# Kernel tuning notes

Hardware: AMD Instinct MI355X
Metric: run time of the kernel (lower is better)

Reference implementation:

```python
import jax, jax.numpy as jnp
import numpy as np

N, C, RATIO, POS_P = 8192, 5000, 3.0, 0.01


def setup_inputs() -> dict:
    key = jax.random.key(0)
    k1, k2 = jax.random.split(key)
    pred = jax.random.normal(k1, (N, C), dtype=jnp.float32)
    # sparse binary multilabel targets (~50 positives per row)
    target = (jax.random.uniform(k2, (N, C)) < POS_P).astype(jnp.float32)
    return {"pred": pred, "target": target}


def reference(pred, target):
    # pred, target: [N, C]
    num_classes = pred.shape[-1]
    pos = jnp.sum(target, axis=-1)                         # [N] positives per row
    neg = jnp.minimum(pos * RATIO, num_classes - pos)      # [N] hard negatives to keep

    # hard-negative selection: top-neg entries of softmax(pred) - target
    prob = jax.nn.softmax(pred, axis=-1)
    score = prob - target                                  # positives pushed below negatives
    # rank 0 = largest score (matches torch.topk ordering)
    ranks = jnp.argsort(jnp.argsort(-score, axis=-1), axis=-1)
    hard = (ranks < neg[:, None]).astype(pred.dtype)       # [N, C]
    mask = jnp.maximum(target, hard)                       # mask = target.clone(); mask[topk]=1

    # old-torch multilabel_soft_margin_loss(size_average=False) == weighted BCE sum:
    # -(y*log sigmoid(x) + (1-y)*log(1-sigmoid(x))) = softplus(x) - y*x
    bce = jax.nn.softplus(pred) - target * pred
    loss = jnp.sum(mask * bce)
    return loss / jnp.sum(target)
```

## Files before the change

### kernel.cpp

```cpp
#include <hip/hip_runtime.h>
#include <stdint.h>


#define C_DIM 5000
#define C4_DIM 1250
#define BLK 256
#define SCAP 1024
#define PCAP 512
#define CUT 1.25f
#define NSLOT 64

__device__ __forceinline__ float sp_f(float x) {
    return fmaxf(x, 0.0f) + __logf(1.0f + __expf(-fabsf(x)));
}
__device__ __forceinline__ uint32_t mono_u(float x) {
    uint32_t b = __float_as_uint(x);
    return b ^ ((b & 0x80000000u) ? 0xFFFFFFFFu : 0x80000000u);
}
__device__ __forceinline__ float unmono_f(uint32_t u) {
    uint32_t b = (u & 0x80000000u) ? (u ^ 0x80000000u) : ~u;
    return __uint_as_float(b);
}
__device__ __forceinline__ int vbin_of(float x) {
    int v = (int)((x - CUT) * 128.0f);
    return v > 255 ? 255 : (v < 0 ? 0 : v);
}

__device__ __forceinline__ void find_bin(const unsigned int* hist, int kp, int tid, int* s_sel) {
    if (tid < 64) {
        int c0 = (int)hist[4 * tid + 0];
        int c1 = (int)hist[4 * tid + 1];
        int c2 = (int)hist[4 * tid + 2];
        int c3 = (int)hist[4 * tid + 3];
        int lsum = c0 + c1 + c2 + c3;
        int s = lsum;
        #pragma unroll
        for (int off = 1; off < 64; off <<= 1) {
            int o = __shfl_down(s, off);
            if (tid + off < 64) s += o;
        }
        int above = s - lsum;
        if (above < kp && kp <= s) {
            int b, ab;
            if (kp <= above + c3)                { b = 4 * tid + 3; ab = above; }
            else if (kp <= above + c3 + c2)      { b = 4 * tid + 2; ab = above + c3; }
            else if (kp <= above + c3 + c2 + c1) { b = 4 * tid + 1; ab = above + c3 + c2; }
            else                                 { b = 4 * tid;     ab = above + c3 + c2 + c1; }
            s_sel[0] = b;
            s_sel[1] = ab;
        }
    }
}

__global__ __launch_bounds__(BLK, 4) void hardneg_kernel(
    const float* __restrict__ pred, const float* __restrict__ target,
    char* __restrict__ ws)
{
    __shared__ uint32_t s_buf[SCAP];
    __shared__ uint32_t s_pbuf[PCAP];
    __shared__ unsigned int hist[256];
    __shared__ float f_scr[4];
    __shared__ int s_sel[2];
    __shared__ int s_misc[4];
    __shared__ int s_cnt;
    __shared__ int s_pcnt;
    __shared__ uint32_t s_tiny[64];

    const int tid = threadIdx.x;
    const int lane = tid & 63;
    const int wv = tid >> 6;
    const int row = blockIdx.x;
    const float4* pr4 = (const float4*)(pred + (size_t)row * C_DIM);
    const float4* tg4 = (const float4*)(target + (size_t)row * C_DIM);

    hist[tid] = 0;
    if (tid < 4) s_misc[tid] = 0;
    if (tid == 0) { s_cnt = 0; s_pcnt = 0; }
    __syncthreads();

    #pragma unroll
    for (int c = 0; c < 5; ++c) {
        int i = tid + c * BLK;
        if (c < 4 || i < C4_DIM) {
            float4 p = pr4[i];
            float4 t = tg4[i];
            float xs[4] = {p.x, p.y, p.z, p.w};
            float ts[4] = {t.x, t.y, t.z, t.w};
            #pragma unroll
            for (int j = 0; j < 4; ++j) {
                float x = xs[j];
                if (ts[j] != 0.0f) {
                    int ip = atomicAdd(&s_pcnt, 1);
                    if (ip < PCAP) s_pbuf[ip] = __float_as_uint(x);
                } else if (x > CUT) {
                    int ic = atomicAdd(&s_cnt, 1);
                    if (ic < SCAP) s_buf[ic] = __float_as_uint(x) ^ 0x80000000u;
                }
            }
        }
    }
    __syncthreads();

    const int pos_total = s_pcnt;
    const int cnt = s_cnt;
    const int k = min(3 * pos_total, C_DIM - pos_total);
    if (k == 0) return;

    float acc = 0.0f;
    if (pos_total <= PCAP) {
        for (int i = tid; i < pos_total; i += BLK) {
            float x = __uint_as_float(s_pbuf[i]);
            acc += sp_f(x) - x;
        }
    } else {
        for (int i = tid; i < C4_DIM; i += BLK) {
            float4 p = pr4[i];
            float4 t = tg4[i];
            float xs[4] = {p.x, p.y, p.z, p.w};
            float ts[4] = {t.x, t.y, t.z, t.w};
            #pragma unroll
            for (int j = 0; j < 4; ++j)
                if (ts[j] != 0.0f) acc += sp_f(xs[j]) - xs[j];
        }
    }

    uint32_t tu;
    int n_at;
    const bool fb = (k > cnt) || (cnt > SCAP);

    if (!fb) {
        for (int i = tid; i < cnt; i += BLK)
            atomicAdd(&hist[vbin_of(unmono_f(s_buf[i]))], 1u);
        __syncthreads();
        find_bin(hist, k, tid, s_sel);
        __syncthreads();
        const int bv = s_sel[0];
        int kp = k - s_sel[1];

        for (int i = tid; i < cnt; i += BLK) {
            uint32_t u = s_buf[i];
            if (vbin_of(unmono_f(u)) == bv) {
                int idx = atomicAdd(&s_misc[0], 1);
                if (idx < 64) s_tiny[idx] = u;
            }
        }
        __syncthreads();
        const int tcnt = s_misc[0];

        if (tcnt <= 64) {
            if (tid < 64) {
                uint32_t ul = (lane < tcnt) ? s_tiny[lane] : 0u;
                int sg = 0, eq = 0;
                for (int j = 0; j < tcnt; ++j) {
                    uint32_t uj = (uint32_t)__shfl((int)ul, j);
                    sg += (uj > ul);
                    eq += (uj == ul);
                }
                if (lane < tcnt && sg < kp && kp <= sg + eq) {
                    s_misc[1] = (int)ul;
                    s_misc[2] = kp - sg;
                }
            }
            __syncthreads();
            tu = (uint32_t)s_misc[1];
            n_at = s_misc[2];
        } else {
            uint32_t prefix = 0;
            for (int r = 0; r < 4; ++r) {
                const int shift = 24 - 8 * r;
                __syncthreads();
                hist[tid] = 0;
                __syncthreads();
                for (int i = tid; i < cnt; i += BLK) {
                    uint32_t u = s_buf[i];
                    bool match = (vbin_of(unmono_f(u)) == bv);
                    if (r > 0) match = match && ((u >> (shift + 8)) == (prefix >> (shift + 8)));
                    if (match) atomicAdd(&hist[(u >> shift) & 255u], 1u);
                }
                __syncthreads();
                find_bin(hist, kp, tid, s_sel);
                __syncthreads();
                prefix |= ((uint32_t)s_sel[0]) << shift;
                kp -= s_sel[1];
            }
            tu = prefix;
            n_at = kp;
        }

        for (int i = tid; i < cnt; i += BLK) {
            uint32_t u = s_buf[i];
            if (u > tu) acc += sp_f(unmono_f(u));
        }
    } else {
        uint32_t prefix = 0;
        int kq = k;
        for (int r = 0; r < 4; ++r) {
            const int shift = 24 - 8 * r;
            __syncthreads();
            hist[tid] = 0;
            __syncthreads();
            for (int i = tid; i < C4_DIM; i += BLK) {
                float4 p = pr4[i];
                float4 t = tg4[i];
                float xs[4] = {p.x, p.y, p.z, p.w};
                float ts[4] = {t.x, t.y, t.z, t.w};
                #pragma unroll
                for (int j = 0; j < 4; ++j) {
                    if (ts[j] == 0.0f) {
                        uint32_t u = mono_u(xs[j]);
                        bool m = (r == 0) || ((u >> (shift + 8)) == (prefix >> (shift + 8)));
                        if (m) atomicAdd(&hist[(u >> shift) & 255u], 1u);
                    }
                }
            }
            __syncthreads();
            find_bin(hist, kq, tid, s_sel);
            __syncthreads();
            prefix |= ((uint32_t)s_sel[0]) << shift;
            kq -= s_sel[1];
        }
        tu = prefix;
        n_at = kq;
        for (int i = tid; i < C4_DIM; i += BLK) {
            float4 p = pr4[i];
            float4 t = tg4[i];
            float xs[4] = {p.x, p.y, p.z, p.w};
            float ts[4] = {t.x, t.y, t.z, t.w};
            #pragma unroll
            for (int j = 0; j < 4; ++j) {
                if (ts[j] == 0.0f && mono_u(xs[j]) > tu) acc += sp_f(xs[j]);
            }
        }
    }

    #pragma unroll
    for (int off = 32; off; off >>= 1) acc += __shfl_down(acc, off);
    if (lane == 0) f_scr[wv] = acc;
    __syncthreads();
    if (tid == 0) {
        float rowsum = f_scr[0] + f_scr[1] + f_scr[2] + f_scr[3]
                     + (float)n_at * sp_f(unmono_f(tu));
        char* slot = ws + (size_t)(row & (NSLOT - 1)) * 16;
        atomicAdd((double*)slot, (double)rowsum);
        atomicAdd((float*)(slot + 8), (float)pos_total);
    }
}

__global__ void hardneg_finalize(const char* __restrict__ ws, float* __restrict__ out)
{
    const int l = threadIdx.x;
    double n = *(const double*)(ws + (size_t)l * 16);
    float d = *(const float*)(ws + (size_t)l * 16 + 8);
    #pragma unroll
    for (int off = 32; off; off >>= 1) {
        n += __shfl_down(n, off);
        d += __shfl_down(d, off);
    }
    if (l == 0) out[0] = (d > 0.0f) ? (float)(n / (double)d) : 0.0f;
}

extern "C" void kernel_launch(void* const* d_in, const int* in_sizes, int n_in,
                              void* d_out, int out_size, void* d_ws, size_t ws_size,
                              hipStream_t stream) {
    const float* pred = (const float*)d_in[0];
    const float* target = (const float*)d_in[1];
    float* out = (float*)d_out;
    char* ws = (char*)d_ws;

    hipMemsetAsync(ws, 0, NSLOT * 16, stream);

    const int nrows = in_sizes[0] / C_DIM;
    hardneg_kernel<<<nrows, BLK, 0, stream>>>(pred, target, ws);
    hardneg_finalize<<<1, 64, 0, stream>>>(ws, out);
}
```

Baseline: 337.2 us.

## Process one row per wavefront with ballot compaction and fused histogram

Changes the work split from one 256-thread block per row to one 64-lane wavefront per row, four rows per block. Block barriers become wave-local LDS waits. Candidate compaction now uses ballot/popcount prefix instead of shared atomics, and the coarse histogram plus the positive-sum are built in the first streaming pass, removing extra passes over the buffer. The aim is to cut barrier and atomic overhead and allow more occupancy, at the cost of less memory parallelism per row. It also relies on nrows being divisible by 4 and on lgkmcnt waits being enough for intra-wave LDS visibility.

```diff
diff --git a/kernel.cpp b/kernel.cpp
--- a/kernel.cpp
+++ b/kernel.cpp
@@ -5,10 +5,11 @@
 #define C_DIM 5000
 #define C4_DIM 1250
 #define BLK 256
-#define SCAP 1024
-#define PCAP 512
+#define WSCAP 768
 #define CUT 1.25f
 #define NSLOT 64
+
+#define WSYNC() asm volatile("s_waitcnt lgkmcnt(0)" ::: "memory")
 
 __device__ __forceinline__ float sp_f(float x) {
     return fmaxf(x, 0.0f) + __logf(1.0f + __expf(-fabsf(x)));
@@ -26,169 +27,163 @@
     return v > 255 ? 255 : (v < 0 ? 0 : v);
 }
 
-__device__ __forceinline__ void find_bin(const unsigned int* hist, int kp, int tid, int* s_sel) {
-    if (tid < 64) {
-        int c0 = (int)hist[4 * tid + 0];
-        int c1 = (int)hist[4 * tid + 1];
-        int c2 = (int)hist[4 * tid + 2];
-        int c3 = (int)hist[4 * tid + 3];
-        int lsum = c0 + c1 + c2 + c3;
-        int s = lsum;
-        #pragma unroll
-        for (int off = 1; off < 64; off <<= 1) {
-            int o = __shfl_down(s, off);
-            if (tid + off < 64) s += o;
-        }
-        int above = s - lsum;
-        if (above < kp && kp <= s) {
-            int b, ab;
-            if (kp <= above + c3)                { b = 4 * tid + 3; ab = above; }
-            else if (kp <= above + c3 + c2)      { b = 4 * tid + 2; ab = above + c3; }
-            else if (kp <= above + c3 + c2 + c1) { b = 4 * tid + 1; ab = above + c3 + c2; }
-            else                                 { b = 4 * tid;     ab = above + c3 + c2 + c1; }
-            s_sel[0] = b;
-            s_sel[1] = ab;
-        }
-    }
-}
-
-__global__ __launch_bounds__(BLK, 4) void hardneg_kernel(
+__device__ __forceinline__ void find_bin_w(const unsigned int* h, int kp, int lane, int* misc) {
+    int c0 = (int)h[4 * lane + 0];
+    int c1 = (int)h[4 * lane + 1];
+    int c2 = (int)h[4 * lane + 2];
+    int c3 = (int)h[4 * lane + 3];
+    int lsum = c0 + c1 + c2 + c3;
+    int s = lsum;
+    #pragma unroll
+    for (int off = 1; off < 64; off <<= 1) {
+        int o = __shfl_down(s, off);
+        if (lane + off < 64) s += o;
+    }
+    int above = s - lsum;
+    if (above < kp && kp <= s) {
+        int b, ab;
+        if (kp <= above + c3)                { b = 4 * lane + 3; ab = above; }
+        else if (kp <= above + c3 + c2)      { b = 4 * lane + 2; ab = above + c3; }
+        else if (kp <= above + c3 + c2 + c1) { b = 4 * lane + 1; ab = above + c3 + c2; }
+        else                                 { b = 4 * lane;     ab = above + c3 + c2 + c1; }
+        misc[0] = b;
+        misc[1] = ab;
+    }
+}
+
+__global__ __launch_bounds__(BLK, 6) void hardneg_kernel(
     const float* __restrict__ pred, const float* __restrict__ target,
     char* __restrict__ ws)
 {
-    __shared__ uint32_t s_buf[SCAP];
-    __shared__ uint32_t s_pbuf[PCAP];
-    __shared__ unsigned int hist[256];
-    __shared__ float f_scr[4];
-    __shared__ int s_sel[2];
-    __shared__ int s_misc[4];
-    __shared__ int s_cnt;
-    __shared__ int s_pcnt;
-    __shared__ uint32_t s_tiny[64];
-
-    const int tid = threadIdx.x;
-    const int lane = tid & 63;
-    const int wv = tid >> 6;
-    const int row = blockIdx.x;
+    __shared__ uint32_t s_buf[4][WSCAP];
+    __shared__ unsigned int s_hist[4][256];
+    __shared__ uint32_t s_tiny[4][64];
+    __shared__ int s_misc[4][4];
+
+    const int lane = threadIdx.x & 63;
+    const int wv = threadIdx.x >> 6;
+    const int row = blockIdx.x * 4 + wv;
+
+    uint32_t* sbuf = s_buf[wv];
+    unsigned int* h = s_hist[wv];
+    int* misc = s_misc[wv];
+
     const float4* pr4 = (const float4*)(pred + (size_t)row * C_DIM);
     const float4* tg4 = (const float4*)(target + (size_t)row * C_DIM);
 
-    hist[tid] = 0;
-    if (tid < 4) s_misc[tid] = 0;
-    if (tid == 0) { s_cnt = 0; s_pcnt = 0; }
-    __syncthreads();
-
-    #pragma unroll
-    for (int c = 0; c < 5; ++c) {
-        int i = tid + c * BLK;
-        if (c < 4 || i < C4_DIM) {
-            float4 p = pr4[i];
-            float4 t = tg4[i];
-            float xs[4] = {p.x, p.y, p.z, p.w};
-            float ts[4] = {t.x, t.y, t.z, t.w};
-            #pragma unroll
-            for (int j = 0; j < 4; ++j) {
-                float x = xs[j];
-                if (ts[j] != 0.0f) {
-                    int ip = atomicAdd(&s_pcnt, 1);
-                    if (ip < PCAP) s_pbuf[ip] = __float_as_uint(x);
-                } else if (x > CUT) {
-                    int ic = atomicAdd(&s_cnt, 1);
-                    if (ic < SCAP) s_buf[ic] = __float_as_uint(x) ^ 0x80000000u;
-                }
-            }
-        }
-    }
-    __syncthreads();
-
-    const int pos_total = s_pcnt;
-    const int cnt = s_cnt;
+    h[lane] = 0; h[lane + 64] = 0; h[lane + 128] = 0; h[lane + 192] = 0;
+    WSYNC();
+
+    float acc = 0.0f;
+    int pcnt = 0;
+    unsigned wcnt = 0;
+    const unsigned long long ltmask = (1ull << lane) - 1ull;
+
+    #define PROC(xv, tv) do {                                                  \
+        float x_ = (xv);                                                       \
+        bool ispos_ = ((tv) != 0.0f);                                          \
+        bool cand_ = (!ispos_) && (x_ > CUT);                                  \
+        unsigned long long m_ = __ballot(cand_);                               \
+        if (cand_) {                                                           \
+            unsigned slot_ = wcnt + (unsigned)__popcll(m_ & ltmask);           \
+            if (slot_ < WSCAP) sbuf[slot_] = __float_as_uint(x_) ^ 0x80000000u;\
+            atomicAdd(&h[vbin_of(x_)], 1u);                                    \
+        }                                                                      \
+        wcnt += (unsigned)__popcll(m_);                                        \
+        if (ispos_) { pcnt++; acc += sp_f(x_) - x_; }                          \
+    } while (0)
+
+    #pragma unroll 4
+    for (int c = 0; c < 19; ++c) {
+        int idx = c * 64 + lane;
+        float4 p = pr4[idx];
+        float4 t = tg4[idx];
+        PROC(p.x, t.x); PROC(p.y, t.y); PROC(p.z, t.z); PROC(p.w, t.w);
+    }
+    {
+        int idx = 19 * 64 + lane;
+        float4 p = {0.f, 0.f, 0.f, 0.f}, t = {0.f, 0.f, 0.f, 0.f};
+        if (idx < C4_DIM) { p = pr4[idx]; t = tg4[idx]; }
+        PROC(p.x, t.x); PROC(p.y, t.y); PROC(p.z, t.z); PROC(p.w, t.w);
+    }
+    #undef PROC
+
+    int pt = pcnt;
+    #pragma unroll
+    for (int off = 32; off; off >>= 1) pt += __shfl_xor(pt, off);
+    const int pos_total = pt;
     const int k = min(3 * pos_total, C_DIM - pos_total);
+    const int cnt = (int)wcnt;
     if (k == 0) return;
 
-    float acc = 0.0f;
-    if (pos_total <= PCAP) {
-        for (int i = tid; i < pos_total; i += BLK) {
-            float x = __uint_as_float(s_pbuf[i]);
-            acc += sp_f(x) - x;
-        }
-    } else {
-        for (int i = tid; i < C4_DIM; i += BLK) {
-            float4 p = pr4[i];
-            float4 t = tg4[i];
-            float xs[4] = {p.x, p.y, p.z, p.w};
-            float ts[4] = {t.x, t.y, t.z, t.w};
-            #pragma unroll
-            for (int j = 0; j < 4; ++j)
-                if (ts[j] != 0.0f) acc += sp_f(xs[j]) - xs[j];
-        }
-    }
+    WSYNC();
 
     uint32_t tu;
     int n_at;
-    const bool fb = (k > cnt) || (cnt > SCAP);
+    const bool fb = (k > cnt) || (cnt > WSCAP);
 
     if (!fb) {
-        for (int i = tid; i < cnt; i += BLK)
-            atomicAdd(&hist[vbin_of(unmono_f(s_buf[i]))], 1u);
-        __syncthreads();
-        find_bin(hist, k, tid, s_sel);
-        __syncthreads();
-        const int bv = s_sel[0];
-        int kp = k - s_sel[1];
-
-        for (int i = tid; i < cnt; i += BLK) {
-            uint32_t u = s_buf[i];
-            if (vbin_of(unmono_f(u)) == bv) {
-                int idx = atomicAdd(&s_misc[0], 1);
-                if (idx < 64) s_tiny[idx] = u;
-            }
-        }
-        __syncthreads();
-        const int tcnt = s_misc[0];
+        find_bin_w(h, k, lane, misc);
+        WSYNC();
+        const int bv = misc[0];
+        const int kp = k - misc[1];
+
+        unsigned tcnt = 0;
+        const int bound = (cnt + 63) & ~63;
+        for (int i = lane; i < bound; i += 64) {
+            bool in = (i < cnt);
+            uint32_t u = in ? sbuf[i] : 0u;
+            bool hit = in && (vbin_of(unmono_f(u)) == bv);
+            unsigned long long m = __ballot(hit);
+            if (hit) {
+                unsigned idx = tcnt + (unsigned)__popcll(m & ltmask);
+                if (idx < 64) s_tiny[wv][idx] = u;
+            }
+            tcnt += (unsigned)__popcll(m);
+        }
+        WSYNC();
 
         if (tcnt <= 64) {
-            if (tid < 64) {
-                uint32_t ul = (lane < tcnt) ? s_tiny[lane] : 0u;
-                int sg = 0, eq = 0;
-                for (int j = 0; j < tcnt; ++j) {
-                    uint32_t uj = (uint32_t)__shfl((int)ul, j);
-                    sg += (uj > ul);
-                    eq += (uj == ul);
-                }
-                if (lane < tcnt && sg < kp && kp <= sg + eq) {
-                    s_misc[1] = (int)ul;
-                    s_misc[2] = kp - sg;
-                }
-            }
-            __syncthreads();
-            tu = (uint32_t)s_misc[1];
-            n_at = s_misc[2];
+            uint32_t ul = (lane < (int)tcnt) ? s_tiny[wv][lane] : 0u;
+            int sg = 0, eq = 0;
+            for (int j = 0; j < (int)tcnt; ++j) {
+                uint32_t uj = (uint32_t)__shfl((int)ul, j);
+                sg += (uj > ul);
+                eq += (uj == ul);
+            }
+            if (lane < (int)tcnt && sg < kp && kp <= sg + eq) {
+                misc[2] = (int)ul;
+                misc[3] = kp - sg;
+            }
+            WSYNC();
+            tu = (uint32_t)misc[2];
+            n_at = misc[3];
         } else {
             uint32_t prefix = 0;
+            int kq = kp;
             for (int r = 0; r < 4; ++r) {
                 const int shift = 24 - 8 * r;
-                __syncthreads();
-                hist[tid] = 0;
-                __syncthreads();
-                for (int i = tid; i < cnt; i += BLK) {
-                    uint32_t u = s_buf[i];
+                WSYNC();
+                h[lane] = 0; h[lane + 64] = 0; h[lane + 128] = 0; h[lane + 192] = 0;
+                WSYNC();
+                for (int i = lane; i < cnt; i += 64) {
+                    uint32_t u = sbuf[i];
                     bool match = (vbin_of(unmono_f(u)) == bv);
                     if (r > 0) match = match && ((u >> (shift + 8)) == (prefix >> (shift + 8)));
-                    if (match) atomicAdd(&hist[(u >> shift) & 255u], 1u);
+                    if (match) atomicAdd(&h[(u >> shift) & 255u], 1u);
                 }
-                __syncthreads();
-                find_bin(hist, kp, tid, s_sel);
-                __syncthreads();
-                prefix |= ((uint32_t)s_sel[0]) << shift;
-                kp -= s_sel[1];
+                WSYNC();
+                find_bin_w(h, kq, lane, misc);
+                WSYNC();
+                prefix |= ((uint32_t)misc[0]) << shift;
+                kq -= misc[1];
             }
             tu = prefix;
-            n_at = kp;
-        }
-
-        for (int i = tid; i < cnt; i += BLK) {
-            uint32_t u = s_buf[i];
+            n_at = kq;
+        }
+
+        for (int i = lane; i < cnt; i += 64) {
+            uint32_t u = sbuf[i];
             if (u > tu) acc += sp_f(unmono_f(u));
         }
     } else {
@@ -196,50 +191,47 @@
         int kq = k;
         for (int r = 0; r < 4; ++r) {
             const int shift = 24 - 8 * r;
-            __syncthreads();
-            hist[tid] = 0;
-            __syncthreads();
-            for (int i = tid; i < C4_DIM; i += BLK) {
+            WSYNC();
+            h[lane] = 0; h[lane + 64] = 0; h[lane + 128] = 0; h[lane + 192] = 0;
+            WSYNC();
+            for (int i = lane; i < C4_DIM; i += 64) {
                 float4 p = pr4[i];
                 float4 t = tg4[i];
                 float xs[4] = {p.x, p.y, p.z, p.w};
-                float ts[4] = {t.x, t.y, t.z, t.w};
+                float tsv[4] = {t.x, t.y, t.z, t.w};
                 #pragma unroll
                 for (int j = 0; j < 4; ++j) {
-                    if (ts[j] == 0.0f) {
+                    if (tsv[j] == 0.0f) {
                         uint32_t u = mono_u(xs[j]);
                         bool m = (r == 0) || ((u >> (shift + 8)) == (prefix >> (shift + 8)));
-                        if (m) atomicAdd(&hist[(u >> shift) & 255u], 1u);
+                        if (m) atomicAdd(&h[(u >> shift) & 255u], 1u);
                     }
                 }
             }
-            __syncthreads();
-            find_bin(hist, kq, tid, s_sel);
-            __syncthreads();
-            prefix |= ((uint32_t)s_sel[0]) << shift;
-            kq -= s_sel[1];
+            WSYNC();
+            find_bin_w(h, kq, lane, misc);
+            WSYNC();
+            prefix |= ((uint32_t)misc[0]) << shift;
+            kq -= misc[1];
         }
         tu = prefix;
         n_at = kq;
-        for (int i = tid; i < C4_DIM; i += BLK) {
+        for (int i = lane; i < C4_DIM; i += 64) {
             float4 p = pr4[i];
             float4 t = tg4[i];
             float xs[4] = {p.x, p.y, p.z, p.w};
-            float ts[4] = {t.x, t.y, t.z, t.w};
+            float tsv[4] = {t.x, t.y, t.z, t.w};
             #pragma unroll
             for (int j = 0; j < 4; ++j) {
-                if (ts[j] == 0.0f && mono_u(xs[j]) > tu) acc += sp_f(xs[j]);
+                if (tsv[j] == 0.0f && mono_u(xs[j]) > tu) acc += sp_f(xs[j]);
             }
         }
     }
 
     #pragma unroll
     for (int off = 32; off; off >>= 1) acc += __shfl_down(acc, off);
-    if (lane == 0) f_scr[wv] = acc;
-    __syncthreads();
-    if (tid == 0) {
-        float rowsum = f_scr[0] + f_scr[1] + f_scr[2] + f_scr[3]
-                     + (float)n_at * sp_f(unmono_f(tu));
+    if (lane == 0) {
+        float rowsum = acc + (float)n_at * sp_f(unmono_f(tu));
         char* slot = ws + (size_t)(row & (NSLOT - 1)) * 16;
         atomicAdd((double*)slot, (double)rowsum);
         atomicAdd((float*)(slot + 8), (float)pos_total);
@@ -270,6 +262,6 @@
     hipMemsetAsync(ws, 0, NSLOT * 16, stream);
 
     const int nrows = in_sizes[0] / C_DIM;
-    hardneg_kernel<<<nrows, BLK, 0, stream>>>(pred, target, ws);
+    hardneg_kernel<<<nrows / 4, BLK, 0, stream>>>(pred, target, ws);
     hardneg_finalize<<<1, 64, 0, stream>>>(ws, out);
 }
```

Result: slower. 351.8 us (+4.3%).

## Replace shared-atomic candidate compaction with per-thread slot buffers and wave reductions

Applied to the files above, without the earlier changes.

Each thread now keeps its candidate negatives and positives in private strided shared-memory slots instead of appending to shared buffers through atomic counters. Totals come from packed wave-shuffle reductions, and positive/candidate detection is fused into a single fma test. This removes contended LDS atomics in the scan phase and raises the launch-bounds occupancy hint. In exchange the per-thread slot caps are small, so rows that overflow fall back to the slow full-row radix path, which is heavier. Partial-sum slots are also widened and spread to reduce global atomic contention.

```diff
diff --git a/kernel.cpp b/kernel.cpp
--- a/kernel.cpp
+++ b/kernel.cpp
@@ -5,10 +5,10 @@
 #define C_DIM 5000
 #define C4_DIM 1250
 #define BLK 256
-#define SCAP 1024
-#define PCAP 512
-#define CUT 1.25f
-#define NSLOT 64
+#define CCAP 10
+#define PCAP 6
+#define CUT 1.5f
+#define NSLOT 128
 
 __device__ __forceinline__ float sp_f(float x) {
     return fmaxf(x, 0.0f) + __logf(1.0f + __expf(-fabsf(x)));
@@ -52,18 +52,17 @@
     }
 }
 
-__global__ __launch_bounds__(BLK, 4) void hardneg_kernel(
+__global__ __launch_bounds__(BLK, 6) void hardneg_kernel(
     const float* __restrict__ pred, const float* __restrict__ target,
     char* __restrict__ ws)
 {
-    __shared__ uint32_t s_buf[SCAP];
-    __shared__ uint32_t s_pbuf[PCAP];
+    __shared__ uint32_t sbuf[CCAP * BLK];
+    __shared__ uint32_t pbuf[PCAP * BLK];
     __shared__ unsigned int hist[256];
+    __shared__ unsigned int w_scr[4];
     __shared__ float f_scr[4];
     __shared__ int s_sel[2];
     __shared__ int s_misc[4];
-    __shared__ int s_cnt;
-    __shared__ int s_pcnt;
     __shared__ uint32_t s_tiny[64];
 
     const int tid = threadIdx.x;
@@ -75,70 +74,66 @@
 
     hist[tid] = 0;
     if (tid < 4) s_misc[tid] = 0;
-    if (tid == 0) { s_cnt = 0; s_pcnt = 0; }
     __syncthreads();
 
-    #pragma unroll
-    for (int c = 0; c < 5; ++c) {
-        int i = tid + c * BLK;
-        if (c < 4 || i < C4_DIM) {
-            float4 p = pr4[i];
-            float4 t = tg4[i];
-            float xs[4] = {p.x, p.y, p.z, p.w};
-            float ts[4] = {t.x, t.y, t.z, t.w};
-            #pragma unroll
-            for (int j = 0; j < 4; ++j) {
-                float x = xs[j];
-                if (ts[j] != 0.0f) {
-                    int ip = atomicAdd(&s_pcnt, 1);
-                    if (ip < PCAP) s_pbuf[ip] = __float_as_uint(x);
-                } else if (x > CUT) {
-                    int ic = atomicAdd(&s_cnt, 1);
-                    if (ic < SCAP) s_buf[ic] = __float_as_uint(x) ^ 0x80000000u;
-                }
-            }
-        }
-    }
+    float4 a0 = pr4[tid];        float4 b0 = tg4[tid];
+    float4 a1 = pr4[tid + 256];  float4 b1 = tg4[tid + 256];
+    float4 a2 = pr4[tid + 512];  float4 b2 = tg4[tid + 512];
+    float4 a3 = pr4[tid + 768];  float4 b3 = tg4[tid + 768];
+    float4 a4 = {0.f, 0.f, 0.f, 0.f}, b4 = {0.f, 0.f, 0.f, 0.f};
+    if (tid < C4_DIM - 1024) { a4 = pr4[tid + 1024]; b4 = tg4[tid + 1024]; }
+
+    int mc = 0, mp = 0;
+    #define PE(xv, tv) do {                                                       \
+        float y_ = fmaf((tv), -512.0f, (xv));                                     \
+        if (y_ > CUT) {                                                           \
+            if (mc < CCAP) sbuf[tid + (mc << 8)] = __float_as_uint(y_) ^ 0x80000000u; \
+            ++mc;                                                                 \
+        } else if (y_ < -100.0f) {                                                \
+            if (mp < PCAP) pbuf[tid + (mp << 8)] = __float_as_uint(xv);           \
+            ++mp;                                                                 \
+        }                                                                         \
+    } while (0)
+
+    PE(a0.x, b0.x); PE(a0.y, b0.y); PE(a0.z, b0.z); PE(a0.w, b0.w);
+    PE(a1.x, b1.x); PE(a1.y, b1.y); PE(a1.z, b1.z); PE(a1.w, b1.w);
+    PE(a2.x, b2.x); PE(a2.y, b2.y); PE(a2.z, b2.z); PE(a2.w, b2.w);
+    PE(a3.x, b3.x); PE(a3.y, b3.y); PE(a3.z, b3.z); PE(a3.w, b3.w);
+    PE(a4.x, b4.x); PE(a4.y, b4.y); PE(a4.z, b4.z); PE(a4.w, b4.w);
+    #undef PE
+
+    if (mc > CCAP || mp > PCAP) atomicOr(&s_misc[3], 1);
+    unsigned pk = (unsigned)mc | ((unsigned)mp << 16);
+    #pragma unroll
+    for (int off = 32; off; off >>= 1) pk += (unsigned)__shfl_xor((int)pk, off);
+    if (lane == 0) w_scr[wv] = pk;
     __syncthreads();
-
-    const int pos_total = s_pcnt;
-    const int cnt = s_cnt;
+    const unsigned tot = w_scr[0] + w_scr[1] + w_scr[2] + w_scr[3];
+    const int cnt = (int)(tot & 0xFFFFu);
+    const int pos_total = (int)(tot >> 16);
     const int k = min(3 * pos_total, C_DIM - pos_total);
     if (k == 0) return;
 
+    const bool fb = (s_misc[3] != 0) || (k > cnt);
     float acc = 0.0f;
-    if (pos_total <= PCAP) {
-        for (int i = tid; i < pos_total; i += BLK) {
-            float x = __uint_as_float(s_pbuf[i]);
-            acc += sp_f(x) - x;
-        }
-    } else {
-        for (int i = tid; i < C4_DIM; i += BLK) {
-            float4 p = pr4[i];
-            float4 t = tg4[i];
-            float xs[4] = {p.x, p.y, p.z, p.w};
-            float ts[4] = {t.x, t.y, t.z, t.w};
-            #pragma unroll
-            for (int j = 0; j < 4; ++j)
-                if (ts[j] != 0.0f) acc += sp_f(xs[j]) - xs[j];
-        }
-    }
-
     uint32_t tu;
     int n_at;
-    const bool fb = (k > cnt) || (cnt > SCAP);
 
     if (!fb) {
-        for (int i = tid; i < cnt; i += BLK)
-            atomicAdd(&hist[vbin_of(unmono_f(s_buf[i]))], 1u);
+        for (int j = 0; j < mp; ++j) {
+            float x = __uint_as_float(pbuf[tid + (j << 8)]);
+            acc += sp_f(x) - x;
+        }
+        for (int j = 0; j < mc; ++j)
+            atomicAdd(&hist[vbin_of(unmono_f(sbuf[tid + (j << 8)]))], 1u);
         __syncthreads();
         find_bin(hist, k, tid, s_sel);
         __syncthreads();
         const int bv = s_sel[0];
-        int kp = k - s_sel[1];
-
-        for (int i = tid; i < cnt; i += BLK) {
-            uint32_t u = s_buf[i];
+        const int kp = k - s_sel[1];
+
+        for (int j = 0; j < mc; ++j) {
+            uint32_t u = sbuf[tid + (j << 8)];
             if (vbin_of(unmono_f(u)) == bv) {
                 int idx = atomicAdd(&s_misc[0], 1);
                 if (idx < 64) s_tiny[idx] = u;
@@ -166,32 +161,34 @@
             n_at = s_misc[2];
         } else {
             uint32_t prefix = 0;
+            int kq = kp;
             for (int r = 0; r < 4; ++r) {
                 const int shift = 24 - 8 * r;
                 __syncthreads();
                 hist[tid] = 0;
                 __syncthreads();
-                for (int i = tid; i < cnt; i += BLK) {
-                    uint32_t u = s_buf[i];
+                for (int j = 0; j < mc; ++j) {
+                    uint32_t u = sbuf[tid + (j << 8)];
                     bool match = (vbin_of(unmono_f(u)) == bv);
                     if (r > 0) match = match && ((u >> (shift + 8)) == (prefix >> (shift + 8)));
                     if (match) atomicAdd(&hist[(u >> shift) & 255u], 1u);
                 }
                 __syncthreads();
-                find_bin(hist, kp, tid, s_sel);
+                find_bin(hist, kq, tid, s_sel);
                 __syncthreads();
                 prefix |= ((uint32_t)s_sel[0]) << shift;
-                kp -= s_sel[1];
+                kq -= s_sel[1];
             }
             tu = prefix;
-            n_at = kp;
-        }
-
-        for (int i = tid; i < cnt; i += BLK) {
-            uint32_t u = s_buf[i];
+            n_at = kq;
+        }
+
+        for (int j = 0; j < mc; ++j) {
+            uint32_t u = sbuf[tid + (j << 8)];
             if (u > tu) acc += sp_f(unmono_f(u));
         }
     } else {
+        acc = 0.0f;
         uint32_t prefix = 0;
         int kq = k;
         for (int r = 0; r < 4; ++r) {
@@ -203,10 +200,10 @@
                 float4 p = pr4[i];
                 float4 t = tg4[i];
                 float xs[4] = {p.x, p.y, p.z, p.w};
-                float ts[4] = {t.x, t.y, t.z, t.w};
+                float tsv[4] = {t.x, t.y, t.z, t.w};
                 #pragma unroll
                 for (int j = 0; j < 4; ++j) {
-                    if (ts[j] == 0.0f) {
+                    if (tsv[j] == 0.0f) {
                         uint32_t u = mono_u(xs[j]);
                         bool m = (r == 0) || ((u >> (shift + 8)) == (prefix >> (shift + 8)));
                         if (m) atomicAdd(&hist[(u >> shift) & 255u], 1u);
@@ -225,10 +222,11 @@
             float4 p = pr4[i];
             float4 t = tg4[i];
             float xs[4] = {p.x, p.y, p.z, p.w};
-            float ts[4] = {t.x, t.y, t.z, t.w};
+            float tsv[4] = {t.x, t.y, t.z, t.w};
             #pragma unroll
             for (int j = 0; j < 4; ++j) {
-                if (ts[j] == 0.0f && mono_u(xs[j]) > tu) acc += sp_f(xs[j]);
+                if (tsv[j] != 0.0f) acc += sp_f(xs[j]) - xs[j];
+                else if (mono_u(xs[j]) > tu) acc += sp_f(xs[j]);
             }
         }
     }
@@ -240,7 +238,7 @@
     if (tid == 0) {
         float rowsum = f_scr[0] + f_scr[1] + f_scr[2] + f_scr[3]
                      + (float)n_at * sp_f(unmono_f(tu));
-        char* slot = ws + (size_t)(row & (NSLOT - 1)) * 16;
+        char* slot = ws + (size_t)(row & (NSLOT - 1)) * 32;
         atomicAdd((double*)slot, (double)rowsum);
         atomicAdd((float*)(slot + 8), (float)pos_total);
     }
@@ -249,8 +247,14 @@
 __global__ void hardneg_finalize(const char* __restrict__ ws, float* __restrict__ out)
 {
     const int l = threadIdx.x;
-    double n = *(const double*)(ws + (size_t)l * 16);
-    float d = *(const float*)(ws + (size_t)l * 16 + 8);
+    double n = 0.0;
+    float d = 0.0f;
+    #pragma unroll
+    for (int s = 0; s < NSLOT / 64; ++s) {
+        const char* slot = ws + (size_t)(s * 64 + l) * 32;
+        n += *(const double*)slot;
+        d += *(const float*)(slot + 8);
+    }
     #pragma unroll
     for (int off = 32; off; off >>= 1) {
         n += __shfl_down(n, off);
@@ -267,7 +271,7 @@
     float* out = (float*)d_out;
     char* ws = (char*)d_ws;
 
-    hipMemsetAsync(ws, 0, NSLOT * 16, stream);
+    hipMemsetAsync(ws, 0, NSLOT * 32, stream);
 
     const int nrows = in_sizes[0] / C_DIM;
     hardneg_kernel<<<nrows, BLK, 0, stream>>>(pred, target, ws);
```

Result: no change. 332.7 us (-1.3%).
